# Optimization experiments

Measured on AMD Instinct MI355X. Metric: run time of the kernel, lower is better.

Reference implementation:

```python
import jax, jax.numpy as jnp
import numpy as np

B, S = 128, 2048
INPUT_DIM, CTX_DIM = 512, 512


def setup_inputs() -> dict:
    key = jax.random.key(0)
    ks = jax.random.split(key, 9)
    s_in = 1.0 / np.sqrt(INPUT_DIM)
    s_ctx = 1.0 / np.sqrt(CTX_DIM)
    s_out = 1.0 / np.sqrt(INPUT_DIM + CTX_DIM)
    inp = {
        "input": jax.random.normal(ks[0], (B, INPUT_DIM), jnp.float32),
        "context": jax.random.normal(ks[1], (B, S, CTX_DIM), jnp.float32),
        "context_mask": jax.random.randint(ks[2], (B, S), 0, 2) > 0,  # True = masked
        # params (torch Linear stores W as [out,in]; we store [in,out] for x @ W)
        "W_in": jax.random.uniform(ks[3], (INPUT_DIM, CTX_DIM), jnp.float32, -s_in, s_in),
        "b_in": jax.random.uniform(ks[4], (CTX_DIM,), jnp.float32, -s_in, s_in),
        "W_ctx": jax.random.uniform(ks[5], (CTX_DIM, CTX_DIM), jnp.float32, -s_ctx, s_ctx),
        "b_ctx": jax.random.uniform(ks[6], (CTX_DIM,), jnp.float32, -s_ctx, s_ctx),
        "w_score": jax.random.uniform(ks[7], (CTX_DIM,), jnp.float32, -s_ctx, s_ctx),
        "W_out": jax.random.uniform(ks[8], (INPUT_DIM + CTX_DIM, INPUT_DIM), jnp.float32, -s_out, s_out),
        "b_out": jax.random.uniform(jax.random.fold_in(key, 99), (INPUT_DIM,), jnp.float32, -s_out, s_out),
    }
    # ensure at least one unmasked position per row (avoid all -inf softmax)
    inp["context_mask"] = inp["context_mask"].at[:, 0].set(False)
    return inp


def reference(input, context, context_mask, W_in, b_in, W_ctx, b_ctx, w_score, W_out, b_out):
    # input: [B, Di], context: [B, S, Dc]
    q = input @ W_in + b_in                              # [B, Dc]
    k = jnp.einsum("bsd,de->bse", context, W_ctx) + b_ctx  # [B, S, Dc]
    # additive score: v^T tanh(q + k)
    scores = jnp.einsum("bsd,d->bs", jnp.tanh(q[:, None, :] + k), w_score)  # [B, S]
    scores = jnp.where(context_mask, -jnp.inf, scores)
    attn = jax.nn.softmax(scores, axis=-1)               # [B, S]
    ctx_vec = jnp.einsum("bs,bsd->bd", attn, context)    # [B, Dc]
    x = jnp.tanh(jnp.concatenate([ctx_vec, input], axis=1) @ W_out + b_out)  # [B, Di]
    return (x, attn)
```

## Files before the change

### kernel.cpp

```cpp
#include <hip/hip_runtime.h>
#include <hip/hip_bf16.h>
#include <math.h>

#define B_  128
#define S_  2048
#define DI  512
#define DC  512

typedef __attribute__((ext_vector_type(8))) __bf16 bf16x8;
typedef __attribute__((ext_vector_type(4))) float  f32x4;
typedef __attribute__((ext_vector_type(8))) unsigned short us8;

__device__ __forceinline__ float fast_tanh(float x) {
    float e = __expf(2.f * x);
    return 1.f - 2.f * __builtin_amdgcn_rcpf(e + 1.f);
}

__device__ __forceinline__ unsigned short f2bf(float f) {
    unsigned int u = __float_as_uint(f);
    u += 0x7FFF + ((u >> 16) & 1);
    return (unsigned short)(u >> 16);
}

__device__ __forceinline__ unsigned int pk2(float a, float b) {
    union { __hip_bfloat162 h; unsigned int u; } c;
    c.h = __float22bfloat162_rn(make_float2(a, b));
    return c.u;
}

__device__ __forceinline__ float bf2f(unsigned int lo16) {
    return __uint_as_float(lo16 << 16);
}

__global__ __launch_bounds__(256) void qb_kernel(
    const float* __restrict__ input, const float* __restrict__ W_in,
    const float* __restrict__ b_in, const float* __restrict__ b_ctx,
    float* __restrict__ qb)
{
    __shared__ float sIn[DI];
    int b = blockIdx.x, t = threadIdx.x;
    for (int i = t; i < DI; i += 256) sIn[i] = input[b * DI + i];
    __syncthreads();
    int e0 = t * 2;
    float a0 = b_in[e0] + b_ctx[e0];
    float a1 = b_in[e0 + 1] + b_ctx[e0 + 1];
    for (int d = 0; d < DI; ++d) {
        float v = sIn[d];
        const float* w = W_in + (size_t)d * DC + e0;
        a0 += v * w[0];
        a1 += v * w[1];
    }
    qb[b * DC + e0] = a0;
    qb[b * DC + e0 + 1] = a1;
}

__global__ __launch_bounds__(256) void wt_kernel(
    const float* __restrict__ W_ctx, unsigned short* __restrict__ WtF)
{
    int tid = blockIdx.x * 256 + threadIdx.x;
    int s   = tid >> 11;
    int rem = tid & 2047;
    int g   = rem >> 6;
    int l   = rem & 63;
    int c   = g * 16 + (l & 15);
    int k0  = s * 32 + (l >> 4) * 8;
    us8 w;
    #pragma unroll
    for (int j = 0; j < 8; ++j)
        w[j] = f2bf(W_ctx[(size_t)(k0 + j) * DC + c]);
    *(us8*)(WtF + (size_t)tid * 8) = w;
}

__global__ __launch_bounds__(512, 4) void score_kernel(
    const float* __restrict__ ctx,
    const unsigned short* __restrict__ WtF,
    const float* __restrict__ qb,
    const float* __restrict__ wsc,
    const int* __restrict__ mask,
    float* __restrict__ scores_ws,
    float* __restrict__ pv_ws,
    float* __restrict__ ml_ws)
{
    __shared__ __align__(16) unsigned short ctxs[64 * 512];
    __shared__ float sred[8][64];
    __shared__ float sp[64];

    const int t = threadIdx.x;
    const int row0 = blockIdx.x * 64;
    const int bidx = row0 >> 11;
    const int lane = t & 63;
    const int w = t >> 6;
    const int lr = lane & 15, half = lane >> 4;

    #pragma unroll
    for (int i = 0; i < 8; ++i) {
        int u = i * 512 + t;
        int r = u >> 6, kg = u & 63;
        const float4* src = (const float4*)(ctx + (size_t)(row0 + r) * DC + kg * 8);
        float4 va = src[0], vb = src[1];
        unsigned int p0 = pk2(va.x, va.y), p1 = pk2(va.z, va.w);
        unsigned int p2 = pk2(vb.x, vb.y), p3 = pk2(vb.z, vb.w);
        uint4 pk = {p0, p1, p2, p3};
        *(uint4*)((char*)ctxs + ((r * 1024 + kg * 16) ^ ((r & 7) << 4))) = pk;
    }
    __syncthreads();

    f32x4 acc[4][4] = {};
    #pragma unroll 2
    for (int s = 0; s < 16; ++s) {
        bf16x8 bfr[4];
        const us8* wsrc = (const us8*)(WtF +
            (((size_t)s * 32 + w * 4) * 64 + lane) * 8);
        #pragma unroll
        for (int fn = 0; fn < 4; ++fn)
            bfr[fn] = *(const bf16x8*)(wsrc + fn * 64);
        bf16x8 af[4];
        #pragma unroll
        for (int fm = 0; fm < 4; ++fm) {
            int r = fm * 16 + lr;
            af[fm] = *(const bf16x8*)((const char*)ctxs +
                        ((r * 1024 + s * 64 + half * 16) ^ ((r & 7) << 4)));
        }
        #pragma unroll
        for (int fm = 0; fm < 4; ++fm)
            #pragma unroll
            for (int fn = 0; fn < 4; ++fn)
                acc[fm][fn] = __builtin_amdgcn_mfma_f32_16x16x32_bf16(
                    af[fm], bfr[fn], acc[fm][fn], 0, 0, 0);
    }

    float wv[4], qv[4];
    #pragma unroll
    for (int fn = 0; fn < 4; ++fn) {
        int j = w * 64 + fn * 16 + lr;
        wv[fn] = wsc[j];
        qv[fn] = qb[bidx * DC + j];
    }
    #pragma unroll
    for (int fm = 0; fm < 4; ++fm) {
        #pragma unroll
        for (int reg = 0; reg < 4; ++reg) {
            float ssum = 0.f;
            #pragma unroll
            for (int fn = 0; fn < 4; ++fn)
                ssum += wv[fn] * fast_tanh(qv[fn] + acc[fm][fn][reg]);
            #pragma unroll
            for (int m = 8; m >= 1; m >>= 1)
                ssum += __shfl_xor(ssum, m, 64);
            if (lr == 0)
                sred[w][fm * 16 + half * 4 + reg] = ssum;
        }
    }
    __syncthreads();

    if (t < 64) {
        float sc = sred[0][t] + sred[1][t] + sred[2][t] + sred[3][t]
                 + sred[4][t] + sred[5][t] + sred[6][t] + sred[7][t];
        if (mask[row0 + t] != 0) sc = -1e30f;
        scores_ws[row0 + t] = sc;
        float mx = sc;
        #pragma unroll
        for (int m = 32; m >= 1; m >>= 1) mx = fmaxf(mx, __shfl_xor(mx, m, 64));
        float pe = __expf(sc - mx);
        sp[t] = pe;
        float ls = pe;
        #pragma unroll
        for (int m = 32; m >= 1; m >>= 1) ls += __shfl_xor(ls, m, 64);
        if (t == 0) {
            ml_ws[blockIdx.x * 2]     = mx;
            ml_ws[blockIdx.x * 2 + 1] = ls;
        }
    }
    __syncthreads();

    float a0 = 0.f;
    #pragma unroll 8
    for (int s = 0; s < 64; ++s) {
        unsigned int u = *(const unsigned short*)
            ((const char*)ctxs + ((s * 1024 + t * 2) ^ ((s & 7) << 4)));
        a0 += sp[s] * bf2f(u);
    }
    pv_ws[(size_t)blockIdx.x * 512 + t] = a0;
}

__global__ __launch_bounds__(256) void combine_kernel(
    const float* __restrict__ pv, const float* __restrict__ ml,
    const float* __restrict__ scores,
    float* __restrict__ ctxv, float* __restrict__ attn)
{
    int b = blockIdx.x, t = threadIdx.x;
    __shared__ float sm[32], sl[32], sw[32];
    if (t < 32) {
        sm[t] = ml[(b * 32 + t) * 2];
        sl[t] = ml[(b * 32 + t) * 2 + 1];
    }
    __syncthreads();
    float mstar = -1e30f;
    #pragma unroll
    for (int i = 0; i < 32; ++i) mstar = fmaxf(mstar, sm[i]);
    if (t < 32) sw[t] = __expf(sm[t] - mstar);
    __syncthreads();
    float L = 0.f;
    #pragma unroll
    for (int i = 0; i < 32; ++i) L += sw[i] * sl[i];
    float invL = 1.f / L;

    int d0 = t * 2;
    float c0 = 0.f, c1 = 0.f;
    #pragma unroll
    for (int i = 0; i < 32; ++i) {
        float w = sw[i];
        const float2 v = *(const float2*)(pv + (size_t)(b * 32 + i) * 512 + d0);
        c0 += w * v.x; c1 += w * v.y;
    }
    ctxv[b * DC + d0]     = c0 * invL;
    ctxv[b * DC + d0 + 1] = c1 * invL;

    for (int s = t; s < S_; s += 256)
        attn[(size_t)b * S_ + s] = __expf(scores[(size_t)b * S_ + s] - mstar) * invL;
}

__global__ __launch_bounds__(256) void out_kernel(
    const float* __restrict__ ctxv, const float* __restrict__ input,
    const float* __restrict__ W_out, const float* __restrict__ b_out,
    float* __restrict__ x)
{
    __shared__ float sc[DC + DI];
    int b = blockIdx.x, t = threadIdx.x;
    for (int i = t; i < DC; i += 256) sc[i] = ctxv[b * DC + i];
    for (int i = t; i < DI; i += 256) sc[DC + i] = input[b * DI + i];
    __syncthreads();
    int e0 = t * 2;
    float a0 = b_out[e0], a1 = b_out[e0 + 1];
    for (int d = 0; d < DC + DI; ++d) {
        float v = sc[d];
        const float* w = W_out + (size_t)d * DI + e0;
        a0 += v * w[0];
        a1 += v * w[1];
    }
    x[b * DI + e0] = fast_tanh(a0);
    x[b * DI + e0 + 1] = fast_tanh(a1);
}

extern "C" void kernel_launch(void* const* d_in, const int* in_sizes, int n_in,
                              void* d_out, int out_size, void* d_ws, size_t ws_size,
                              hipStream_t stream) {
    const float* input = (const float*)d_in[0];
    const float* ctx   = (const float*)d_in[1];
    const int*   mask  = (const int*)d_in[2];
    const float* W_in  = (const float*)d_in[3];
    const float* b_in  = (const float*)d_in[4];
    const float* W_ctx = (const float*)d_in[5];
    const float* b_ctx = (const float*)d_in[6];
    const float* wsc   = (const float*)d_in[7];
    const float* W_out = (const float*)d_in[8];
    const float* b_out = (const float*)d_in[9];

    float* x_out = (float*)d_out;
    float* attn  = (float*)d_out + B_ * DI;

    const int NBLK = (B_ * S_) / 64;

    char* ws = (char*)d_ws;
    float* qb = (float*)ws;                    ws += (size_t)B_ * DC * 4;
    unsigned short* WtF = (unsigned short*)ws; ws += (size_t)DC * DC * 2;
    float* scores_ws = (float*)ws;             ws += (size_t)B_ * S_ * 4;
    float* pv_ws = (float*)ws;                 ws += (size_t)NBLK * 512 * 4;
    float* ml_ws = (float*)ws;                 ws += (size_t)NBLK * 2 * 4;
    float* ctxv = (float*)ws;                  ws += (size_t)B_ * DC * 4;

    qb_kernel<<<B_, 256, 0, stream>>>(input, W_in, b_in, b_ctx, qb);
    wt_kernel<<<(16 * 32 * 64) / 256, 256, 0, stream>>>(W_ctx, WtF);
    score_kernel<<<NBLK, 512, 0, stream>>>(ctx, WtF, qb, wsc, mask,
                                           scores_ws, pv_ws, ml_ws);
    combine_kernel<<<B_, 256, 0, stream>>>(pv_ws, ml_ws, scores_ws, ctxv, attn);
    out_kernel<<<B_, 256, 0, stream>>>(ctxv, input, W_out, b_out, x_out);
}
```

Baseline: 284.9 us.

## Make score kernel persistent with double-buffered context prefetch; split small GEMVs

The score kernel becomes persistent: 256 blocks of 1024 threads each walk 16 tiles, loading the next 64-row context tile into registers while MFMAs run on the current tile, then storing it into a second LDS buffer. This aims to hide global-load latency, which the one-shot tile-per-block layout exposed. The qb and out GEMV kernels are split over a second grid dimension and a reduction dimension to raise parallelism. In exchange, LDS use doubles to 128KB+ per block, which limits occupancy, and the kernel adds more barriers per tile.

```diff
diff --git a/kernel.cpp b/kernel.cpp
--- a/kernel.cpp
+++ b/kernel.cpp
@@ -38,20 +38,22 @@
     float* __restrict__ qb)
 {
     __shared__ float sIn[DI];
-    int b = blockIdx.x, t = threadIdx.x;
+    __shared__ float part[2][128];
+    int b = blockIdx.x, cg = blockIdx.y, t = threadIdx.x;
     for (int i = t; i < DI; i += 256) sIn[i] = input[b * DI + i];
     __syncthreads();
-    int e0 = t * 2;
-    float a0 = b_in[e0] + b_ctx[e0];
-    float a1 = b_in[e0 + 1] + b_ctx[e0 + 1];
-    for (int d = 0; d < DI; ++d) {
-        float v = sIn[d];
-        const float* w = W_in + (size_t)d * DC + e0;
-        a0 += v * w[0];
-        a1 += v * w[1];
-    }
-    qb[b * DC + e0] = a0;
-    qb[b * DC + e0 + 1] = a1;
+    int e = cg * 128 + (t & 127);
+    int dh = t >> 7;
+    float a = 0.f;
+    const float* wp = W_in + (size_t)(dh * 256) * DC + e;
+    #pragma unroll 4
+    for (int d = 0; d < 256; ++d) a += sIn[dh * 256 + d] * wp[(size_t)d * DC];
+    part[dh][t & 127] = a;
+    __syncthreads();
+    if (t < 128) {
+        int ee = cg * 128 + t;
+        qb[b * DC + ee] = b_in[ee] + b_ctx[ee] + part[0][t] + part[1][t];
+    }
 }
 
 __global__ __launch_bounds__(256) void wt_kernel(
@@ -71,7 +73,7 @@
     *(us8*)(WtF + (size_t)tid * 8) = w;
 }
 
-__global__ __launch_bounds__(512, 4) void score_kernel(
+__global__ __launch_bounds__(1024, 4) void score_kernel(
     const float* __restrict__ ctx,
     const unsigned short* __restrict__ WtF,
     const float* __restrict__ qb,
@@ -81,106 +83,149 @@
     float* __restrict__ pv_ws,
     float* __restrict__ ml_ws)
 {
-    __shared__ __align__(16) unsigned short ctxs[64 * 512];
+    __shared__ __align__(16) unsigned short ctxs[2][64 * 512];
     __shared__ float sred[8][64];
     __shared__ float sp[64];
+    __shared__ float pvpart[2][512];
 
     const int t = threadIdx.x;
-    const int row0 = blockIdx.x * 64;
-    const int bidx = row0 >> 11;
     const int lane = t & 63;
     const int w = t >> 6;
+    const int wr = w >> 3;
+    const int wcol = w & 7;
     const int lr = lane & 15, half = lane >> 4;
 
-    #pragma unroll
-    for (int i = 0; i < 8; ++i) {
-        int u = i * 512 + t;
-        int r = u >> 6, kg = u & 63;
-        const float4* src = (const float4*)(ctx + (size_t)(row0 + r) * DC + kg * 8);
-        float4 va = src[0], vb = src[1];
-        unsigned int p0 = pk2(va.x, va.y), p1 = pk2(va.z, va.w);
-        unsigned int p2 = pk2(vb.x, vb.y), p3 = pk2(vb.z, vb.w);
-        uint4 pk = {p0, p1, p2, p3};
-        *(uint4*)((char*)ctxs + ((r * 1024 + kg * 16) ^ ((r & 7) << 4))) = pk;
-    }
-    __syncthreads();
-
-    f32x4 acc[4][4] = {};
-    #pragma unroll 2
-    for (int s = 0; s < 16; ++s) {
-        bf16x8 bfr[4];
-        const us8* wsrc = (const us8*)(WtF +
-            (((size_t)s * 32 + w * 4) * 64 + lane) * 8);
+    float4 va[4], vb[4];
+
+    {
+        const int row0 = blockIdx.x * 64;
         #pragma unroll
-        for (int fn = 0; fn < 4; ++fn)
-            bfr[fn] = *(const bf16x8*)(wsrc + fn * 64);
-        bf16x8 af[4];
+        for (int i = 0; i < 4; ++i) {
+            const float4* src = (const float4*)(ctx + (size_t)(row0 + i * 16 + w) * DC + lane * 8);
+            va[i] = src[0]; vb[i] = src[1];
+        }
         #pragma unroll
-        for (int fm = 0; fm < 4; ++fm) {
-            int r = fm * 16 + lr;
-            af[fm] = *(const bf16x8*)((const char*)ctxs +
-                        ((r * 1024 + s * 64 + half * 16) ^ ((r & 7) << 4)));
-        }
+        for (int i = 0; i < 4; ++i) {
+            int r = i * 16 + w;
+            uint4 pk4 = {pk2(va[i].x, va[i].y), pk2(va[i].z, va[i].w),
+                         pk2(vb[i].x, vb[i].y), pk2(vb[i].z, vb[i].w)};
+            *(uint4*)((char*)ctxs[0] + ((r * 1024 + lane * 16) ^ ((r & 7) << 4))) = pk4;
+        }
+    }
+    __syncthreads();
+
+    int cur = 0;
+    #pragma unroll 1
+    for (int it = 0; it < 16; ++it) {
+        const int tile = blockIdx.x + it * 256;
+        const int row0 = tile * 64;
+        const int bidx = row0 >> 11;
+
+        if (it < 15) {
+            const int nrow0 = row0 + 256 * 64;
+            #pragma unroll
+            for (int i = 0; i < 4; ++i) {
+                const float4* src = (const float4*)(ctx + (size_t)(nrow0 + i * 16 + w) * DC + lane * 8);
+                va[i] = src[0]; vb[i] = src[1];
+            }
+        }
+
+        f32x4 acc[2][4] = {};
+        #pragma unroll 2
+        for (int s = 0; s < 16; ++s) {
+            bf16x8 bfr[4];
+            const us8* wsrc = (const us8*)(WtF + (((size_t)s * 32 + wcol * 4) * 64 + lane) * 8);
+            #pragma unroll
+            for (int fn = 0; fn < 4; ++fn)
+                bfr[fn] = *(const bf16x8*)(wsrc + fn * 64);
+            bf16x8 af[2];
+            #pragma unroll
+            for (int fm = 0; fm < 2; ++fm) {
+                int r = wr * 32 + fm * 16 + lr;
+                af[fm] = *(const bf16x8*)((const char*)ctxs[cur] +
+                            ((r * 1024 + s * 64 + half * 16) ^ ((r & 7) << 4)));
+            }
+            #pragma unroll
+            for (int fm = 0; fm < 2; ++fm)
+                #pragma unroll
+                for (int fn = 0; fn < 4; ++fn)
+                    acc[fm][fn] = __builtin_amdgcn_mfma_f32_16x16x32_bf16(
+                        af[fm], bfr[fn], acc[fm][fn], 0, 0, 0);
+        }
+
+        if (it < 15) {
+            #pragma unroll
+            for (int i = 0; i < 4; ++i) {
+                int r = i * 16 + w;
+                uint4 pk4 = {pk2(va[i].x, va[i].y), pk2(va[i].z, va[i].w),
+                             pk2(vb[i].x, vb[i].y), pk2(vb[i].z, vb[i].w)};
+                *(uint4*)((char*)ctxs[cur ^ 1] + ((r * 1024 + lane * 16) ^ ((r & 7) << 4))) = pk4;
+            }
+        }
+
+        float wv[4], qv[4];
         #pragma unroll
-        for (int fm = 0; fm < 4; ++fm)
-            #pragma unroll
-            for (int fn = 0; fn < 4; ++fn)
-                acc[fm][fn] = __builtin_amdgcn_mfma_f32_16x16x32_bf16(
-                    af[fm], bfr[fn], acc[fm][fn], 0, 0, 0);
-    }
-
-    float wv[4], qv[4];
-    #pragma unroll
-    for (int fn = 0; fn < 4; ++fn) {
-        int j = w * 64 + fn * 16 + lr;
-        wv[fn] = wsc[j];
-        qv[fn] = qb[bidx * DC + j];
-    }
-    #pragma unroll
-    for (int fm = 0; fm < 4; ++fm) {
+        for (int fn = 0; fn < 4; ++fn) {
+            int j = wcol * 64 + fn * 16 + lr;
+            wv[fn] = wsc[j];
+            qv[fn] = qb[bidx * DC + j];
+        }
         #pragma unroll
-        for (int reg = 0; reg < 4; ++reg) {
-            float ssum = 0.f;
-            #pragma unroll
-            for (int fn = 0; fn < 4; ++fn)
-                ssum += wv[fn] * fast_tanh(qv[fn] + acc[fm][fn][reg]);
-            #pragma unroll
-            for (int m = 8; m >= 1; m >>= 1)
-                ssum += __shfl_xor(ssum, m, 64);
-            if (lr == 0)
-                sred[w][fm * 16 + half * 4 + reg] = ssum;
-        }
-    }
-    __syncthreads();
-
-    if (t < 64) {
-        float sc = sred[0][t] + sred[1][t] + sred[2][t] + sred[3][t]
-                 + sred[4][t] + sred[5][t] + sred[6][t] + sred[7][t];
-        if (mask[row0 + t] != 0) sc = -1e30f;
-        scores_ws[row0 + t] = sc;
-        float mx = sc;
-        #pragma unroll
-        for (int m = 32; m >= 1; m >>= 1) mx = fmaxf(mx, __shfl_xor(mx, m, 64));
-        float pe = __expf(sc - mx);
-        sp[t] = pe;
-        float ls = pe;
-        #pragma unroll
-        for (int m = 32; m >= 1; m >>= 1) ls += __shfl_xor(ls, m, 64);
-        if (t == 0) {
-            ml_ws[blockIdx.x * 2]     = mx;
-            ml_ws[blockIdx.x * 2 + 1] = ls;
-        }
-    }
-    __syncthreads();
-
-    float a0 = 0.f;
-    #pragma unroll 8
-    for (int s = 0; s < 64; ++s) {
-        unsigned int u = *(const unsigned short*)
-            ((const char*)ctxs + ((s * 1024 + t * 2) ^ ((s & 7) << 4)));
-        a0 += sp[s] * bf2f(u);
-    }
-    pv_ws[(size_t)blockIdx.x * 512 + t] = a0;
+        for (int fm = 0; fm < 2; ++fm) {
+            #pragma unroll
+            for (int reg = 0; reg < 4; ++reg) {
+                float ssum = 0.f;
+                #pragma unroll
+                for (int fn = 0; fn < 4; ++fn)
+                    ssum += wv[fn] * fast_tanh(qv[fn] + acc[fm][fn][reg]);
+                #pragma unroll
+                for (int m = 8; m >= 1; m >>= 1)
+                    ssum += __shfl_xor(ssum, m, 64);
+                if (lr == 0)
+                    sred[wcol][wr * 32 + fm * 16 + half * 4 + reg] = ssum;
+            }
+        }
+        __syncthreads();
+
+        if (t < 64) {
+            float sc = sred[0][t] + sred[1][t] + sred[2][t] + sred[3][t]
+                     + sred[4][t] + sred[5][t] + sred[6][t] + sred[7][t];
+            if (mask[row0 + t] != 0) sc = -1e30f;
+            scores_ws[row0 + t] = sc;
+            float mx = sc;
+            #pragma unroll
+            for (int m = 32; m >= 1; m >>= 1) mx = fmaxf(mx, __shfl_xor(mx, m, 64));
+            float pe = __expf(sc - mx);
+            sp[t] = pe;
+            float ls = pe;
+            #pragma unroll
+            for (int m = 32; m >= 1; m >>= 1) ls += __shfl_xor(ls, m, 64);
+            if (t == 0) {
+                ml_ws[tile * 2]     = mx;
+                ml_ws[tile * 2 + 1] = ls;
+            }
+        }
+        __syncthreads();
+
+        {
+            int col = t & 511, rh = t >> 9;
+            float a0 = 0.f;
+            #pragma unroll 8
+            for (int s2 = 0; s2 < 32; ++s2) {
+                int r = rh * 32 + s2;
+                unsigned int u = *(const unsigned short*)
+                    ((const char*)ctxs[cur] + ((r * 1024 + col * 2) ^ ((r & 7) << 4)));
+                a0 += sp[r] * bf2f(u);
+            }
+            pvpart[rh][col] = a0;
+        }
+        __syncthreads();
+        if (t < 512)
+            pv_ws[(size_t)tile * 512 + t] = pvpart[0][t] + pvpart[1][t];
+
+        __syncthreads();
+        cur ^= 1;
+    }
 }
 
 __global__ __launch_bounds__(256) void combine_kernel(
@@ -225,21 +270,24 @@
     const float* __restrict__ W_out, const float* __restrict__ b_out,
     float* __restrict__ x)
 {
-    __shared__ float sc[DC + DI];
-    int b = blockIdx.x, t = threadIdx.x;
-    for (int i = t; i < DC; i += 256) sc[i] = ctxv[b * DC + i];
-    for (int i = t; i < DI; i += 256) sc[DC + i] = input[b * DI + i];
-    __syncthreads();
-    int e0 = t * 2;
-    float a0 = b_out[e0], a1 = b_out[e0 + 1];
-    for (int d = 0; d < DC + DI; ++d) {
-        float v = sc[d];
-        const float* w = W_out + (size_t)d * DI + e0;
-        a0 += v * w[0];
-        a1 += v * w[1];
-    }
-    x[b * DI + e0] = fast_tanh(a0);
-    x[b * DI + e0 + 1] = fast_tanh(a1);
+    __shared__ float scm[DC + DI];
+    __shared__ float part[2][128];
+    int b = blockIdx.x, cg = blockIdx.y, t = threadIdx.x;
+    for (int i = t; i < DC; i += 256) scm[i] = ctxv[b * DC + i];
+    for (int i = t; i < DI; i += 256) scm[DC + i] = input[b * DI + i];
+    __syncthreads();
+    int e = cg * 128 + (t & 127);
+    int dh = t >> 7;
+    float a = 0.f;
+    const float* wp = W_out + (size_t)(dh * 512) * DI + e;
+    #pragma unroll 4
+    for (int d = 0; d < 512; ++d) a += scm[dh * 512 + d] * wp[(size_t)d * DI];
+    part[dh][t & 127] = a;
+    __syncthreads();
+    if (t < 128) {
+        int ee = cg * 128 + t;
+        x[b * DI + ee] = fast_tanh(b_out[ee] + part[0][t] + part[1][t]);
+    }
 }
 
 extern "C" void kernel_launch(void* const* d_in, const int* in_sizes, int n_in,
@@ -259,20 +307,20 @@
     float* x_out = (float*)d_out;
     float* attn  = (float*)d_out + B_ * DI;
 
-    const int NBLK = (B_ * S_) / 64;
+    const int NTILE = (B_ * S_) / 64;
 
     char* ws = (char*)d_ws;
     float* qb = (float*)ws;                    ws += (size_t)B_ * DC * 4;
     unsigned short* WtF = (unsigned short*)ws; ws += (size_t)DC * DC * 2;
     float* scores_ws = (float*)ws;             ws += (size_t)B_ * S_ * 4;
-    float* pv_ws = (float*)ws;                 ws += (size_t)NBLK * 512 * 4;
-    float* ml_ws = (float*)ws;                 ws += (size_t)NBLK * 2 * 4;
+    float* pv_ws = (float*)ws;                 ws += (size_t)NTILE * 512 * 4;
+    float* ml_ws = (float*)ws;                 ws += (size_t)NTILE * 2 * 4;
     float* ctxv = (float*)ws;                  ws += (size_t)B_ * DC * 4;
 
-    qb_kernel<<<B_, 256, 0, stream>>>(input, W_in, b_in, b_ctx, qb);
+    qb_kernel<<<dim3(B_, 4), 256, 0, stream>>>(input, W_in, b_in, b_ctx, qb);
     wt_kernel<<<(16 * 32 * 64) / 256, 256, 0, stream>>>(W_ctx, WtF);
-    score_kernel<<<NBLK, 512, 0, stream>>>(ctx, WtF, qb, wsc, mask,
+    score_kernel<<<256, 1024, 0, stream>>>(ctx, WtF, qb, wsc, mask,
                                            scores_ws, pv_ws, ml_ws);
     combine_kernel<<<B_, 256, 0, stream>>>(pv_ws, ml_ws, scores_ws, ctxv, attn);
-    out_kernel<<<B_, 256, 0, stream>>>(ctxv, input, W_out, b_out, x_out);
-}
+    out_kernel<<<dim3(B_, 4), 256, 0, stream>>>(ctxv, input, W_out, b_out, x_out);
+}
```

Result: slower. 467.0 us (+63.9%).
